# Kernel optimization log

Measured on AMD Instinct MI355X. Metric: run time of the kernel, lower is better.

Reference implementation:

```python
import jax, jax.numpy as jnp
import numpy as np

BINS = 7
NUM_CLASSES = 21
SCALE = 0.0625


def _psroi_pool_mean(x, rois, batch_idx, bins, scale):
    """Position-sensitive RoI average pool (torchvision PSRoIPool semantics)
    followed by mean over the bins x bins grid.
    x: [N, Cg*bins*bins, H, W]  rois: [R,4] (x1,y1,x2,y2)  batch_idx: [R] int
    returns [R, Cg].
    Implemented with a summed-area table: bin boundaries are integers, so each
    bin sum is 4 corner lookups -> avoids materializing per-RoI feature crops.
    """
    N, C, H, W = x.shape
    Cg = C // (bins * bins)
    # channel layout: c_in = (c_out * bins + i) * bins + j
    xr = x.reshape(N, Cg, bins, bins, H, W)
    sat = jnp.cumsum(jnp.cumsum(xr, axis=-2), axis=-1)
    sat = jnp.pad(sat, ((0, 0), (0, 0), (0, 0), (0, 0), (1, 0), (1, 0)))
    # -> [N, bins_i, bins_j, H+1, W+1, Cg] so advanced indexing yields [R,bins,bins,Cg]
    sat = jnp.transpose(sat, (0, 2, 3, 4, 5, 1))

    # round-half-away-from-zero (coords are non-negative)
    x1 = jnp.floor(rois[:, 0] * scale + 0.5).astype(jnp.int32)
    y1 = jnp.floor(rois[:, 1] * scale + 0.5).astype(jnp.int32)
    x2 = jnp.floor(rois[:, 2] * scale + 0.5).astype(jnp.int32)
    y2 = jnp.floor(rois[:, 3] * scale + 0.5).astype(jnp.int32)
    roi_w = jnp.maximum(x2 - x1, 1).astype(jnp.float32)
    roi_h = jnp.maximum(y2 - y1, 1).astype(jnp.float32)
    bw = roi_w / bins  # [R]
    bh = roi_h / bins
    k = jnp.arange(bins, dtype=jnp.float32)
    wstart = jnp.clip(jnp.floor(k[None, :] * bw[:, None]).astype(jnp.int32) + x1[:, None], 0, W)  # [R,bins]
    wend = jnp.clip(jnp.ceil((k[None, :] + 1.0) * bw[:, None]).astype(jnp.int32) + x1[:, None], 0, W)
    hstart = jnp.clip(jnp.floor(k[None, :] * bh[:, None]).astype(jnp.int32) + y1[:, None], 0, H)
    hend = jnp.clip(jnp.ceil((k[None, :] + 1.0) * bh[:, None]).astype(jnp.int32) + y1[:, None], 0, H)

    b = batch_idx.astype(jnp.int32)
    ii = jnp.arange(bins)[None, :, None]
    jj = jnp.arange(bins)[None, None, :]

    def corner(hh, ww):  # hh,ww: [R,bins] -> [R,bins,bins,Cg]
        return sat[b[:, None, None], ii, jj, hh[:, :, None], ww[:, None, :]]

    s = corner(hend, wend) - corner(hstart, wend) - corner(hend, wstart) + corner(hstart, wstart)
    area = ((hend - hstart)[:, :, None] * (wend - wstart)[:, None, :])  # [R,bins,bins] int
    areaf = jnp.maximum(area, 1).astype(x.dtype)
    pooled = jnp.where((area <= 0)[..., None], 0.0, s / areaf[..., None])  # [R,bins,bins,Cg]
    return pooled.mean(axis=(1, 2))  # [R, Cg]


def setup_inputs() -> dict:
    key = jax.random.key(0)
    ks = jax.random.split(key, 6)
    N, C_in, H, W = 2, 1024, 64, 64
    R = 1024
    h = jax.random.normal(ks[0], (N, C_in, H, W), dtype=jnp.float32)
    pt = jax.random.uniform(ks[1], (R, 2), minval=0.0, maxval=800.0)
    sz = jax.random.uniform(ks[2], (R, 2), minval=32.0, maxval=224.0)
    rois = jnp.concatenate([pt, jnp.minimum(pt + sz, 1023.0)], axis=1).astype(jnp.float32)
    roi_indices = jax.random.randint(ks[3], (R,), 0, N, dtype=jnp.int32)
    Wc = 0.01 * jax.random.normal(ks[4], (BINS * BINS * NUM_CLASSES, C_in), dtype=jnp.float32)
    bc = jnp.zeros((BINS * BINS * NUM_CLASSES,), jnp.float32)
    Wl = 0.01 * jax.random.normal(ks[5], (BINS * BINS * 4 * NUM_CLASSES, C_in), dtype=jnp.float32)
    bl = jnp.zeros((BINS * BINS * 4 * NUM_CLASSES,), jnp.float32)
    return {"h": h, "rois": rois, "roi_indices": roi_indices, "Wc": Wc, "bc": bc, "Wl": Wl, "bl": bl}


def reference(h, rois, roi_indices, Wc, bc, Wl, bl):
    # roi_extractor = identity; 1x1 convs are channel matmuls
    h_cls = jnp.einsum('nchw,oc->nohw', h, Wc) + bc[None, :, None, None]
    h_reg = jnp.einsum('nchw,oc->nohw', h, Wl) + bl[None, :, None, None]
    roi_score = _psroi_pool_mean(h_cls, rois, roi_indices, BINS, SCALE)  # [R, num_classes]
    roi_locs = _psroi_pool_mean(h_reg, rois, roi_indices, BINS, SCALE)  # [R, 4*num_classes]
    return roi_score, roi_locs
```

## Files before the change

kernel.cpp:

```cpp
#include <hip/hip_runtime.h>
#include <math.h>

#define NBIN 49
#define NOUT 105
#define NCLS 21
#define BM 64
#define BK 64
#define MTILES 16

typedef __attribute__((ext_vector_type(4))) float f32x4;
typedef __attribute__((ext_vector_type(8))) short bf16x8;

__device__ __forceinline__ unsigned short bf16rne(float x) {
  unsigned u = __float_as_uint(x);
  u = (u + 0x7FFFu + ((u >> 16) & 1u)) >> 16;
  return (unsigned short)u;
}

__global__ __launch_bounds__(256) void k_transpose(const float* __restrict__ h,
                                                   float* __restrict__ hT) {
  __shared__ float tile[32][33];
  const int b  = blockIdx.z;
  const int s0 = blockIdx.x * 32;
  const int c0 = blockIdx.y * 32;
  const int tx = threadIdx.x & 31, ty = threadIdx.x >> 5;
#pragma unroll
  for (int i = 0; i < 4; ++i) {
    int c = c0 + ty + i * 8;
    tile[ty + i * 8][tx] = h[((size_t)b * 1024 + c) * 4096 + s0 + tx];
  }
  __syncthreads();
#pragma unroll
  for (int i = 0; i < 4; ++i) {
    int s = s0 + ty + i * 8;
    hT[((size_t)b * 4096 + s) * 1024 + c0 + tx] = tile[tx][ty + i * 8];
  }
}

__global__ __launch_bounds__(256) void k_ycumsum(float* __restrict__ hT) {
  const int c = blockIdx.x * 256 + threadIdx.x;
  const int x = blockIdx.y;
  const int b = blockIdx.z;
  float* p = hT + ((size_t)b * 4096 + x) * 1024 + c;
  float run = 0.f;
#pragma unroll 4
  for (int y = 0; y < 64; ++y) {
    run += p[(size_t)y * 65536];
    p[(size_t)y * 65536] = run;
  }
}

__global__ __launch_bounds__(256) void k_pool_gemm(
    const float* __restrict__ Y, const float* __restrict__ rois,
    const int* __restrict__ ridx, const float* __restrict__ Wc,
    const float* __restrict__ bc, const float* __restrict__ Wl,
    const float* __restrict__ bl, float* out) {
  const int mt  = blockIdx.x;
  const int bin = blockIdx.y;
  const int bi = bin / 7, bj = bin % 7;
  const int t = threadIdx.x;

  __shared__ unsigned short AsS[BM * BK];
  __shared__ unsigned short WlS[(NOUT + 7) * BK];
  __shared__ int   wsS[BM], weS[BM], hiS[BM], loS[BM], bS[BM];
  __shared__ float scS[BM], mkS[BM], lsS[BM];

  if (t < BM) {
    int r = mt * BM + t;
    int x1 = (int)floorf(rois[r * 4 + 0] * 0.0625f + 0.5f);
    int y1 = (int)floorf(rois[r * 4 + 1] * 0.0625f + 0.5f);
    int x2 = (int)floorf(rois[r * 4 + 2] * 0.0625f + 0.5f);
    int y2 = (int)floorf(rois[r * 4 + 3] * 0.0625f + 0.5f);
    const float INV7 = 1.0f / 7.0f;
    float bw = (float)max(x2 - x1, 1) * INV7;
    float bh = (float)max(y2 - y1, 1) * INV7;
    int ws_ = min(max((int)floorf((float)bj * bw) + x1, 0), 64);
    int we_ = min(max((int)ceilf((float)(bj + 1) * bw) + x1, 0), 64);
    int hs_ = min(max((int)floorf((float)bi * bh) + y1, 0), 64);
    int he_ = min(max((int)ceilf((float)(bi + 1) * bh) + y1, 0), 64);
    int area = (he_ - hs_) * (we_ - ws_);
    bool m = area > 0;
    scS[t] = m ? 1.0f / (49.0f * (float)area) : 0.0f;
    mkS[t] = m ? (1.0f / 49.0f) : 0.0f;
    wsS[t] = ws_;
    weS[t] = m ? we_ : ws_;
    hiS[t] = m ? (he_ - 1) * 64 : 0;
    loS[t] = max(hs_ - 1, 0) * 64;
    lsS[t] = (hs_ > 0) ? 1.0f : 0.0f;
    bS[t]  = ridx[r];
  }
  __syncthreads();

  const int tx = t & 15, ty = t >> 4;
  const int ty4 = ty * 4;
  const int w = t >> 6;
  const int l = t & 63;
  const int lrow = l & 15, lk8 = (l >> 4) * 8;

  f32x4 acc[7];
#pragma unroll
  for (int nt = 0; nt < 7; ++nt) acc[nt] = (f32x4){0.f, 0.f, 0.f, 0.f};

  for (int c0 = 0; c0 < 1024; c0 += BK) {
#pragma unroll
    for (int rr = 0; rr < 4; ++rr) {
      int r = ty4 + rr;
      float s0 = 0.f, s1 = 0.f, s2 = 0.f, s3 = 0.f;
      const int ws = wsS[r], we = weS[r], hi = hiS[r], lo = loS[r];
      const float ls = lsS[r];
      const float* baseY = Y + (size_t)bS[r] * 4096 * 1024 + c0 + tx * 4;
      for (int x = ws; x < we; ++x) {
        const float4 vh = *(const float4*)&baseY[(size_t)(hi + x) * 1024];
        const float4 vl = *(const float4*)&baseY[(size_t)(lo + x) * 1024];
        s0 += vh.x - ls * vl.x;
        s1 += vh.y - ls * vl.y;
        s2 += vh.z - ls * vl.z;
        s3 += vh.w - ls * vl.w;
      }
      float sc = scS[r];
      unsigned p0 = (unsigned)bf16rne(s0 * sc) | ((unsigned)bf16rne(s1 * sc) << 16);
      unsigned p1 = (unsigned)bf16rne(s2 * sc) | ((unsigned)bf16rne(s3 * sc) << 16);
      int idx = (r * BK + tx * 4) ^ ((r & 7) << 3);
      *(uint2*)&AsS[idx] = make_uint2(p0, p1);
    }
#pragma unroll
    for (int it = 0; it < 7; ++it) {
      int idx = t + it * 256;
      int row = idx >> 4;
      int cq  = idx & 15;
      float4 v = {0.f, 0.f, 0.f, 0.f};
      if (row < NCLS)
        v = *(const float4*)&Wc[(size_t)(row * 49 + bin) * 1024 + c0 + cq * 4];
      else if (row < NOUT)
        v = *(const float4*)&Wl[(size_t)((row - NCLS) * 49 + bin) * 1024 + c0 + cq * 4];
      unsigned p0 = (unsigned)bf16rne(v.x) | ((unsigned)bf16rne(v.y) << 16);
      unsigned p1 = (unsigned)bf16rne(v.z) | ((unsigned)bf16rne(v.w) << 16);
      int widx = (row * BK + cq * 4) ^ ((row & 7) << 3);
      *(uint2*)&WlS[widx] = make_uint2(p0, p1);
    }
    __syncthreads();

    bf16x8 af[2];
#pragma unroll
    for (int ks = 0; ks < 2; ++ks) {
      int r = w * 16 + lrow;
      int k = ks * 32 + lk8;
      int ai = (r * BK + k) ^ ((r & 7) << 3);
      af[ks] = *(const bf16x8*)&AsS[ai];
    }
#pragma unroll
    for (int nt = 0; nt < 7; ++nt) {
#pragma unroll
      for (int ks = 0; ks < 2; ++ks) {
        int row = nt * 16 + lrow;
        int k = ks * 32 + lk8;
        int bix = (row * BK + k) ^ ((row & 7) << 3);
        bf16x8 bf = *(const bf16x8*)&WlS[bix];
        acc[nt] = __builtin_amdgcn_mfma_f32_16x16x32_bf16(af[ks], bf, acc[nt], 0, 0, 0);
      }
    }
    __syncthreads();
  }

#pragma unroll
  for (int nt = 0; nt < 7; ++nt) {
    int o = nt * 16 + (l & 15);
    if (o < NOUT) {
      float bias = (o < NCLS) ? bc[o * 49 + bin] : bl[(o - NCLS) * 49 + bin];
#pragma unroll
      for (int b = 0; b < 4; ++b) {
        int r_loc = w * 16 + 4 * (l >> 4) + b;
        int gr = mt * BM + r_loc;
        float val = acc[nt][b] + mkS[r_loc] * bias;
        if (o < NCLS)
          atomicAdd(&out[gr * NCLS + o], val);
        else
          atomicAdd(&out[1024 * NCLS + gr * 84 + (o - NCLS)], val);
      }
    }
  }
}

extern "C" void kernel_launch(void* const* d_in, const int* in_sizes, int n_in,
                              void* d_out, int out_size, void* d_ws, size_t ws_size,
                              hipStream_t stream) {
  const float* h    = (const float*)d_in[0];
  const float* rois = (const float*)d_in[1];
  const int*   ridx = (const int*)d_in[2];
  const float* Wc   = (const float*)d_in[3];
  const float* bc   = (const float*)d_in[4];
  const float* Wl   = (const float*)d_in[5];
  const float* bl   = (const float*)d_in[6];
  float* out = (float*)d_out;

  float* hT = (float*)d_ws;

  hipMemsetAsync(out, 0, (size_t)out_size * sizeof(float), stream);
  k_transpose<<<dim3(128, 32, 2), 256, 0, stream>>>(h, hT);
  k_ycumsum<<<dim3(4, 64, 2), 256, 0, stream>>>(hT);
  k_pool_gemm<<<dim3(MTILES, NBIN), 256, 0, stream>>>(hT, rois, ridx, Wc, bc, Wl, bl, out);
}
```

Baseline: 165.8 us.

## Prepack weights to swizzled bf16 and remap blocks so each XCD shares bins

Adds a kernel that converts Wc/Wl to bf16 once, already in the swizzled LDS tile layout. The pool-GEMM then copies those tiles straight into shared memory instead of reloading fp32 weights and converting them in every M-tile block. The grid is flattened to 1D and remapped so that blocks sharing a bin land on the same XCD, which should improve L2 reuse of the summed-area data and the weights. The cost is an extra launch and workspace use, with the old path kept as a fallback when the workspace is too small. Padded block IDs where the bin is 49 or more simply exit.

```diff
diff --git a/kernel.cpp b/kernel.cpp
--- a/kernel.cpp
+++ b/kernel.cpp
@@ -6,10 +6,12 @@
 #define NCLS 21
 #define BM 64
 #define BK 64
-#define MTILES 16
 
 typedef __attribute__((ext_vector_type(4))) float f32x4;
 typedef __attribute__((ext_vector_type(8))) short bf16x8;
+
+#define YBYTES  33554432u
+#define WPBYTES 11239424u
 
 __device__ __forceinline__ unsigned short bf16rne(float x) {
   unsigned u = __float_as_uint(x);
@@ -50,13 +52,39 @@
   }
 }
 
+__global__ __launch_bounds__(256) void k_wpack(const float* __restrict__ Wc,
+                                               const float* __restrict__ Wl,
+                                               unsigned short* __restrict__ Wp) {
+  const int bin = blockIdx.x, chunk = blockIdx.y, t = threadIdx.x;
+  const int c0 = chunk * 64;
+  unsigned short* dst = Wp + (size_t)(bin * 16 + chunk) * 7168;
+#pragma unroll
+  for (int i = 0; i < 7; ++i) {
+    int idx = t + i * 256;
+    int row = idx >> 4;
+    int cq  = idx & 15;
+    float4 v = {0.f, 0.f, 0.f, 0.f};
+    if (row < NCLS)
+      v = *(const float4*)&Wc[(size_t)(row * 49 + bin) * 1024 + c0 + cq * 4];
+    else if (row < NOUT)
+      v = *(const float4*)&Wl[(size_t)((row - NCLS) * 49 + bin) * 1024 + c0 + cq * 4];
+    unsigned p0 = (unsigned)bf16rne(v.x) | ((unsigned)bf16rne(v.y) << 16);
+    unsigned p1 = (unsigned)bf16rne(v.z) | ((unsigned)bf16rne(v.w) << 16);
+    *(uint2*)&dst[(row * BK + cq * 4) ^ ((row & 7) << 3)] = make_uint2(p0, p1);
+  }
+}
+
 __global__ __launch_bounds__(256) void k_pool_gemm(
     const float* __restrict__ Y, const float* __restrict__ rois,
     const int* __restrict__ ridx, const float* __restrict__ Wc,
     const float* __restrict__ bc, const float* __restrict__ Wl,
-    const float* __restrict__ bl, float* out) {
-  const int mt  = blockIdx.x;
-  const int bin = blockIdx.y;
+    const float* __restrict__ bl, const unsigned short* __restrict__ Wp,
+    const int useWp, float* out) {
+  const int id = blockIdx.x;
+  const int xcd = id & 7, j = id >> 3;
+  const int g = j >> 4, mt = j & 15;
+  const int bin = xcd + (g << 3);
+  if (bin >= NBIN) return;
   const int bi = bin / 7, bj = bin % 7;
   const int t = threadIdx.x;
 
@@ -101,7 +129,8 @@
 #pragma unroll
   for (int nt = 0; nt < 7; ++nt) acc[nt] = (f32x4){0.f, 0.f, 0.f, 0.f};
 
-  for (int c0 = 0; c0 < 1024; c0 += BK) {
+  for (int c0i = 0; c0i < 16; ++c0i) {
+    const int c0 = c0i * 64;
 #pragma unroll
     for (int rr = 0; rr < 4; ++rr) {
       int r = ty4 + rr;
@@ -123,20 +152,29 @@
       int idx = (r * BK + tx * 4) ^ ((r & 7) << 3);
       *(uint2*)&AsS[idx] = make_uint2(p0, p1);
     }
-#pragma unroll
-    for (int it = 0; it < 7; ++it) {
-      int idx = t + it * 256;
-      int row = idx >> 4;
-      int cq  = idx & 15;
-      float4 v = {0.f, 0.f, 0.f, 0.f};
-      if (row < NCLS)
-        v = *(const float4*)&Wc[(size_t)(row * 49 + bin) * 1024 + c0 + cq * 4];
-      else if (row < NOUT)
-        v = *(const float4*)&Wl[(size_t)((row - NCLS) * 49 + bin) * 1024 + c0 + cq * 4];
-      unsigned p0 = (unsigned)bf16rne(v.x) | ((unsigned)bf16rne(v.y) << 16);
-      unsigned p1 = (unsigned)bf16rne(v.z) | ((unsigned)bf16rne(v.w) << 16);
-      int widx = (row * BK + cq * 4) ^ ((row & 7) << 3);
-      *(uint2*)&WlS[widx] = make_uint2(p0, p1);
+    if (useWp) {
+      const uint2* srcW = (const uint2*)(Wp + (size_t)(bin * 16 + c0i) * 7168);
+#pragma unroll
+      for (int i = 0; i < 7; ++i) {
+        int idx = t + i * 256;
+        *(uint2*)&WlS[idx * 4] = srcW[idx];
+      }
+    } else {
+#pragma unroll
+      for (int it = 0; it < 7; ++it) {
+        int idx = t + it * 256;
+        int row = idx >> 4;
+        int cq  = idx & 15;
+        float4 v = {0.f, 0.f, 0.f, 0.f};
+        if (row < NCLS)
+          v = *(const float4*)&Wc[(size_t)(row * 49 + bin) * 1024 + c0 + cq * 4];
+        else if (row < NOUT)
+          v = *(const float4*)&Wl[(size_t)((row - NCLS) * 49 + bin) * 1024 + c0 + cq * 4];
+        unsigned p0 = (unsigned)bf16rne(v.x) | ((unsigned)bf16rne(v.y) << 16);
+        unsigned p1 = (unsigned)bf16rne(v.z) | ((unsigned)bf16rne(v.w) << 16);
+        int widx = (row * BK + cq * 4) ^ ((row & 7) << 3);
+        *(uint2*)&WlS[widx] = make_uint2(p0, p1);
+      }
     }
     __syncthreads();
 
@@ -194,9 +232,13 @@
   float* out = (float*)d_out;
 
   float* hT = (float*)d_ws;
+  unsigned short* Wp = (unsigned short*)((char*)d_ws + YBYTES);
+  const int useWp = (ws_size >= (size_t)YBYTES + WPBYTES) ? 1 : 0;
 
   hipMemsetAsync(out, 0, (size_t)out_size * sizeof(float), stream);
+  if (useWp) k_wpack<<<dim3(NBIN, 16), 256, 0, stream>>>(Wc, Wl, Wp);
   k_transpose<<<dim3(128, 32, 2), 256, 0, stream>>>(h, hT);
   k_ycumsum<<<dim3(4, 64, 2), 256, 0, stream>>>(hT);
-  k_pool_gemm<<<dim3(MTILES, NBIN), 256, 0, stream>>>(hT, rois, ridx, Wc, bc, Wl, bl, out);
-}
+  k_pool_gemm<<<dim3(896), 256, 0, stream>>>(hT, rois, ridx, Wc, bc, Wl, bl,
+                                             Wp, useWp, out);
+}
```

Result: slower. 215.5 us (+30.0%).
